# Kernel tuning notes

Hardware: AMD Instinct MI355X
Metric: run time of the kernel (lower is better)

Reference implementation:

```python
import jax, jax.numpy as jnp
import numpy as np

N_NODES = 50000
N_EDGES = 800000
NUM_RELS = 16
IN_DIM = 16      # == NUM_RELS (one-hot of op_class_id)
H_DIM = 128
OUT_DIM = 128    # must equal H_DIM (actor/critic consume output-layer root feats)
LIN_DIM = 512


def setup_inputs() -> dict:
    key = jax.random.key(0)
    ks = jax.random.split(key, 16)
    op_class_id = jax.random.randint(ks[0], (N_NODES,), 0, NUM_RELS, dtype=jnp.int32)
    norm = jax.random.uniform(ks[1], (N_NODES,), dtype=jnp.float32)
    src = jax.random.randint(ks[2], (N_EDGES,), 0, N_NODES, dtype=jnp.int32)
    dst = jax.random.randint(ks[3], (N_EDGES,), 0, N_NODES, dtype=jnp.int32)
    s = 0.1
    W0 = jax.random.normal(ks[4], (NUM_RELS, IN_DIM, H_DIM), jnp.float32) * s
    W1 = jax.random.normal(ks[5], (NUM_RELS, H_DIM, H_DIM), jnp.float32) * s
    W2 = jax.random.normal(ks[6], (NUM_RELS, H_DIM, OUT_DIM), jnp.float32) * s
    a1_w = jax.random.normal(ks[7], (OUT_DIM, LIN_DIM), jnp.float32) * s
    a1_b = jnp.zeros((LIN_DIM,), jnp.float32)
    a2_w = jax.random.normal(ks[8], (LIN_DIM, OUT_DIM), jnp.float32) * s
    a2_b = jnp.zeros((OUT_DIM,), jnp.float32)
    c1_w = jax.random.normal(ks[9], (OUT_DIM, LIN_DIM), jnp.float32) * s
    c1_b = jnp.zeros((LIN_DIM,), jnp.float32)
    c2_w = jax.random.normal(ks[10], (LIN_DIM, 1), jnp.float32) * s
    c2_b = jnp.zeros((1,), jnp.float32)
    return dict(op_class_id=op_class_id, norm=norm, src=src, dst=dst,
                W0=W0, W1=W1, W2=W2,
                a1_w=a1_w, a1_b=a1_b, a2_w=a2_w, a2_b=a2_b,
                c1_w=c1_w, c1_b=c1_b, c2_w=c2_w, c2_b=c2_b)


def _rgcn_layer(h, cls, norm, src, dst, W, act):
    # per-node relation-specific transform: h[n] @ W[cls[n]]
    # compute all relations then select (R small, avoids [N,in,out] gather)
    stacked = jnp.einsum('ni,rio->rno', h, W)          # [R, N, out]
    msg = stacked[cls, jnp.arange(h.shape[0])]         # [N, out]
    msg = msg * norm[:, None]
    agg = jax.ops.segment_sum(msg[src], dst, num_segments=h.shape[0])
    return act(agg)


def reference(op_class_id, norm, src, dst, W0, W1, W2,
              a1_w, a1_b, a2_w, a2_b, c1_w, c1_b, c2_w, c2_b):
    one_hot = jax.nn.one_hot(op_class_id, IN_DIM, dtype=jnp.float32)  # op_class_one_hot
    h = _rgcn_layer(one_hot, op_class_id, norm, src, dst, W0, jax.nn.relu)
    h = _rgcn_layer(h, op_class_id, norm, src, dst, W1, jax.nn.relu)
    h = _rgcn_layer(h, op_class_id, norm, src, dst, W2,
                    lambda x: jax.nn.softmax(x, axis=1))
    root = h[0]                                        # [OUT_DIM]
    probs = jax.nn.relu(root @ a1_w + a1_b) @ a2_w + a2_b
    value = jax.nn.relu(root @ c1_w + c1_b) @ c2_w + c2_b
    return probs, value
```

## Files before the change

kernel.cpp:

```cpp
#include <hip/hip_runtime.h>

#define NN 50000
#define NE 800000
#define NQ (NE / 4)
#define NR 16
#define HD 128
#define LIND 512

#define E0CAP 4096
#define SEGN 16
#define SEGCAP 2048
#define S1MAX 64
#define BMW 1600

#define PZ ((int)0xAAAAAAAA)

#define CNT(i) cnt[(i) * 16]
#define L_E0      0
#define L_E1(s)   (1 + (s))
#define L_SCAN(s) (17 + (s))
#define L_EDGE(s) (33 + (s))
#define L_DONE    49

#define NEB 256
#define NTB (NEB + NR + 16)

__global__ void k_scanA(const int* __restrict__ src, const int* __restrict__ dst,
                        int* map1, int* e0_src, int* cnt, int* map0bm) {
    int tid = blockIdx.x * blockDim.x + threadIdx.x;
    if (tid >= NQ) {
        int idx = tid - NQ;
        if (idx < BMW) map0bm[idx] = 0;
        return;
    }
    int4 d4 = ((const int4*)dst)[tid];
    int ds[4] = {d4.x, d4.y, d4.z, d4.w};
    #pragma unroll
    for (int j = 0; j < 4; j++) {
        if (ds[j] == 0) {
            int s = src[4 * tid + j];
            int i = atomicAdd(&CNT(L_E0), 1) - PZ;
            if (i >= 0 && i < E0CAP) e0_src[i] = s;
            map1[s] = 1;
        }
    }
}

__global__ void k_scanB1(const int* __restrict__ src, const int* __restrict__ dst,
                         const int* __restrict__ cls, const float* __restrict__ norm,
                         const int* __restrict__ map1, const int* __restrict__ e0_src,
                         int* map0bm, int4* e1seg, int* cnt) {
    __shared__ int s1l[S1MAX];
    int e0n = CNT(L_E0) - PZ;
    if (e0n < 0) e0n = 0; if (e0n > E0CAP) e0n = E0CAP;
    const int s1n = (e0n <= S1MAX) ? e0n : 0;
    if (threadIdx.x < s1n) s1l[threadIdx.x] = e0_src[threadIdx.x];
    __syncthreads();
    int tid = blockIdx.x * blockDim.x + threadIdx.x;
    if (tid >= NQ) return;
    int seg = blockIdx.x & (SEGN - 1);
    int4 d4 = ((const int4*)dst)[tid];
    int ds[4] = {d4.x, d4.y, d4.z, d4.w};
    #pragma unroll
    for (int j = 0; j < 4; j++) {
        int dv = ds[j];
        bool hit;
        if (s1n) {
            hit = false;
            for (int s2 = 0; s2 < s1n; s2++) hit |= (dv == s1l[s2]);
        } else {
            hit = (map1[dv] == 1);
        }
        if (hit) {
            int s = src[4 * tid + j];
            int i = atomicAdd(&CNT(L_E1(seg)), 1) - PZ;
            if (i >= 0 && i < SEGCAP)
                e1seg[seg * SEGCAP + i] =
                    make_int4(s, dv, cls[s], __float_as_int(norm[s]));
            atomicOr(&map0bm[s >> 5], 1 << (s & 31));
        }
    }
}

__global__ void __launch_bounds__(256, 2)
k_tail6(const int* __restrict__ src, const int* __restrict__ dst,
        const int* __restrict__ cls, const float* __restrict__ norm,
        const int* __restrict__ map0bm, int* cnt,
        const int* __restrict__ e0_src, const int4* __restrict__ e1seg,
        float* w0sum, float* agg1, float* rootpre,
        const float* __restrict__ W0, const float* __restrict__ W1,
        const float* __restrict__ W2,
        const float* __restrict__ a1w, const float* __restrict__ a1b,
        const float* __restrict__ a2w, const float* __restrict__ a2b,
        const float* __restrict__ c1w, const float* __restrict__ c1b,
        const float* __restrict__ c2w, const float* __restrict__ c2b,
        float* out) {
    const int t = threadIdx.x;
    const int b = blockIdx.x;

    __shared__ union {
        int bm[BMW];
        struct { float shw[NR]; float sha[HD]; float red[256]; } ed;
        struct { float u[HD]; int si[256]; int sc[256]; float sn[256]; int any; } rt;
        struct { float sha[HD]; float shz[64]; float red[256]; } mlp;
    } sm;

    {
        for (int i = t; i < BMW; i += 256) sm.bm[i] = map0bm[i];
        __syncthreads();
        const int4* d4p = (const int4*)dst;
        for (int q = b * 256 + t; q < NQ; q += NTB * 256) {
            int4 d4 = d4p[q];
            int ds[4] = {d4.x, d4.y, d4.z, d4.w};
            #pragma unroll
            for (int j = 0; j < 4; j++) {
                int dv = ds[j];
                if ((sm.bm[dv >> 5] >> (dv & 31)) & 1) {
                    int s = src[4 * q + j];
                    atomicAdd(&w0sum[((size_t)dv << 4) + cls[s]], norm[s]);
                }
            }
        }
    }
    __syncthreads();
    if (t == 0)
        __hip_atomic_fetch_add(&CNT(L_SCAN(b & (SEGN - 1))), 1,
                               __ATOMIC_RELAXED, __HIP_MEMORY_SCOPE_AGENT);

    if (b < NEB) {
        const int seg = b & (SEGN - 1);
        const int own = b >> 4;
        int len = CNT(L_E1(seg)) - PZ;
        if (len < 0) len = 0; if (len > SEGCAP) len = SEGCAP;
        const int o = t & 127, hf = t >> 7, kk0 = hf << 6;
        int u = 0, v = 0, c = 0; float nm = 0.f;
        float w1reg[64];
        float w0reg[NR];
        if (t < HD) {
            #pragma unroll
            for (int cc = 0; cc < NR; cc++) w0reg[cc] = W0[cc * 2176 + t];
        }
        bool have = (own < len);
        if (have) {
            int4 e = e1seg[seg * SEGCAP + own];
            u = e.x; v = e.y; c = e.z; nm = __int_as_float(e.w);
            const float* w = W1 + c * (HD * HD) + o;
            #pragma unroll
            for (int k = 0; k < 64; k++) w1reg[k] = w[(kk0 + k) << 7];
        }
        if (t == 0) {
            for (;;) {
                int tot = 0;
                #pragma unroll
                for (int s2 = 0; s2 < SEGN; s2++)
                    tot += __hip_atomic_load(&CNT(L_SCAN(s2)), __ATOMIC_RELAXED,
                                             __HIP_MEMORY_SCOPE_AGENT) - PZ;
                if (tot >= NTB) break;
                __builtin_amdgcn_s_sleep(1);
            }
        }
        __syncthreads();
        for (int i = own; i < len; i += NEB / SEGN) {
            if (i != own) {
                int4 e = e1seg[seg * SEGCAP + i];
                u = e.x; v = e.y; c = e.z; nm = __int_as_float(e.w);
                const float* w = W1 + c * (HD * HD) + o;
                #pragma unroll
                for (int k = 0; k < 64; k++) w1reg[k] = w[(kk0 + k) << 7];
            }
            if (t < NR)
                sm.ed.shw[t] = __hip_atomic_load(&w0sum[((size_t)u << 4) + t],
                                                 __ATOMIC_RELAXED,
                                                 __HIP_MEMORY_SCOPE_AGENT);
            __syncthreads();
            if (t < HD) {
                float a = 0.f;
                #pragma unroll
                for (int cc = 0; cc < NR; cc++) a = fmaf(sm.ed.shw[cc], w0reg[cc], a);
                sm.ed.sha[t] = fmaxf(a, 0.f);
            }
            __syncthreads();
            {
                float acc = 0.f;
                #pragma unroll
                for (int k = 0; k < 64; k++)
                    acc = fmaf(sm.ed.sha[kk0 + k], w1reg[k], acc);
                sm.ed.red[t] = acc;
            }
            __syncthreads();
            if (t < HD)
                atomicAdd(&agg1[((size_t)v << 7) + t],
                          (sm.ed.red[t] + sm.ed.red[t + 128]) * nm);
            __syncthreads();
        }
        __syncthreads();
        if (t == 0)
            __hip_atomic_fetch_add(&CNT(L_EDGE(seg)), 1,
                                   __ATOMIC_RELAXED, __HIP_MEMORY_SCOPE_AGENT);
    } else if (b < NEB + NR) {
        const int c = b - NEB;
        const int o = t & 127, hf = t >> 7, kk0 = hf << 6;
        if (t < HD) sm.rt.u[t] = 0.f;
        if (t == 0) sm.rt.any = 0;
        int e0n = CNT(L_E0) - PZ;
        if (e0n < 0) e0n = 0; if (e0n > E0CAP) e0n = E0CAP;
        if (t < e0n && t < 256) {
            int s0 = e0_src[t];
            sm.rt.si[t] = s0; sm.rt.sc[t] = cls[s0]; sm.rt.sn[t] = norm[s0];
        }
        float w2reg[64];
        {
            const float* w2 = W2 + c * (HD * HD) + o;
            #pragma unroll
            for (int k = 0; k < 64; k++) w2reg[k] = w2[(kk0 + k) << 7];
        }
        __syncthreads();
        if (t == 0) {
            for (;;) {
                int tot = 0;
                #pragma unroll
                for (int s2 = 0; s2 < SEGN; s2++)
                    tot += __hip_atomic_load(&CNT(L_EDGE(s2)), __ATOMIC_RELAXED,
                                             __HIP_MEMORY_SCOPE_AGENT) - PZ;
                if (tot >= NEB) break;
                __builtin_amdgcn_s_sleep(1);
            }
        }
        __syncthreads();
        for (int base = 0; base < e0n; base += 256) {
            int nchunk = e0n - base; if (nchunk > 256) nchunk = 256;
            if (base > 0) {
                if (t < nchunk) {
                    int s0 = e0_src[base + t];
                    sm.rt.si[t] = s0; sm.rt.sc[t] = cls[s0]; sm.rt.sn[t] = norm[s0];
                }
                __syncthreads();
            }
            for (int i = 0; i < nchunk; i++) {
                if (sm.rt.sc[i] != c) continue;
                if (t < HD) {
                    float av = __hip_atomic_load(&agg1[((size_t)sm.rt.si[i] << 7) + t],
                                                 __ATOMIC_RELAXED,
                                                 __HIP_MEMORY_SCOPE_AGENT);
                    sm.rt.u[t] += sm.rt.sn[i] * fmaxf(av, 0.f);
                }
                if (t == 0) sm.rt.any = 1;
            }
            __syncthreads();
        }
        if (sm.rt.any) {
            float acc = 0.f;
            #pragma unroll
            for (int k = 0; k < 64; k++) acc = fmaf(sm.rt.u[kk0 + k], w2reg[k], acc);
            atomicAdd(&rootpre[o], acc);
        }
        __syncthreads();
        if (t == 0)
            __hip_atomic_fetch_add(&CNT(L_DONE), 1,
                                   __ATOMIC_RELEASE, __HIP_MEMORY_SCOPE_AGENT);
    } else {
        const int bb = b - NEB - NR;
        const int m = bb >> 3, g = bb & 7, k0 = g << 6;
        const float* Wh = m ? c1w : a1w;
        const float* bh = m ? c1b : a1b;
        const int o1 = t & 63, qu = t >> 6, kk1 = qu << 5;
        float wreg[32];
        #pragma unroll
        for (int i = 0; i < 32; i++) wreg[i] = Wh[(kk1 + i) * LIND + k0 + o1];
        float breg = bh[k0 + o1];
        const int o2 = t & 127, hf2 = t >> 7, j2 = hf2 << 5;
        float vreg[32];
        if (m == 0) {
            #pragma unroll
            for (int j = 0; j < 32; j++) vreg[j] = a2w[(k0 + j2 + j) * HD + o2];
        } else {
            vreg[0] = c2w[k0 + o1];
        }
        if (t == 0) {
            while (__hip_atomic_load(&CNT(L_DONE), __ATOMIC_ACQUIRE,
                                     __HIP_MEMORY_SCOPE_AGENT) - PZ < NR)
                __builtin_amdgcn_s_sleep(2);
        }
        __syncthreads();
        if (t < HD)
            sm.mlp.sha[t] = __hip_atomic_load(&rootpre[t], __ATOMIC_RELAXED,
                                              __HIP_MEMORY_SCOPE_AGENT);
        __syncthreads();
        float mx = -3.0e38f;
        for (int i = 0; i < HD; i++) mx = fmaxf(mx, sm.mlp.sha[i]);
        float ex = (t < HD) ? expf(sm.mlp.sha[t] - mx) : 0.f;
        __syncthreads();
        if (t < HD) sm.mlp.sha[t] = ex;
        __syncthreads();
        float sum = 0.f;
        for (int i = 0; i < HD; i++) sum += sm.mlp.sha[i];
        __syncthreads();
        if (t < HD) sm.mlp.sha[t] = ex / sum;
        __syncthreads();
        {
            float z = 0.f;
            #pragma unroll
            for (int i = 0; i < 32; i++) z = fmaf(sm.mlp.sha[kk1 + i], wreg[i], z);
            sm.mlp.red[t] = z;
            __syncthreads();
            if (t < 64)
                sm.mlp.shz[t] = fmaxf(breg + sm.mlp.red[t] + sm.mlp.red[t + 64]
                                      + sm.mlp.red[t + 128] + sm.mlp.red[t + 192], 0.f);
        }
        __syncthreads();
        if (m == 0) {
            float acc = 0.f;
            #pragma unroll
            for (int j = 0; j < 32; j++) acc = fmaf(sm.mlp.shz[j2 + j], vreg[j], acc);
            sm.mlp.red[t] = acc;
            __syncthreads();
            if (t < HD) {
                float v = sm.mlp.red[t] + sm.mlp.red[t + 128];
                if (bb == 0) v += a2b[t];
                atomicAdd(&out[t], v);
            }
        } else {
            if (t < 64) sm.mlp.red[t] = sm.mlp.shz[t] * vreg[0];
            __syncthreads();
            if (t == 0) {
                float v = (bb == 8) ? c2b[0] : 0.f;
                for (int j = 0; j < 64; j++) v += sm.mlp.red[j];
                atomicAdd(&out[HD], v);
            }
        }
    }
}

extern "C" void kernel_launch(void* const* d_in, const int* in_sizes, int n_in,
                              void* d_out, int out_size, void* d_ws, size_t ws_size,
                              hipStream_t stream) {
    const int*   cls  = (const int*)d_in[0];
    const float* norm = (const float*)d_in[1];
    const int*   src  = (const int*)d_in[2];
    const int*   dst  = (const int*)d_in[3];
    const float* W0   = (const float*)d_in[4];
    const float* W1   = (const float*)d_in[5];
    const float* W2   = (const float*)d_in[6];
    const float* a1w  = (const float*)d_in[7];
    const float* a1b  = (const float*)d_in[8];
    const float* a2w  = (const float*)d_in[9];
    const float* a2b  = (const float*)d_in[10];
    const float* c1w  = (const float*)d_in[11];
    const float* c1b  = (const float*)d_in[12];
    const float* c2w  = (const float*)d_in[13];
    const float* c2b  = (const float*)d_in[14];
    float* out = (float*)d_out;

    char*  ws      = (char*)d_ws;
    int*   cnt     = (int*)(ws + 0);
    int*   e0_src  = (int*)(ws + 4096);
    float* rootpre = (float*)(ws + 20480);
    int*   map0bm  = (int*)(ws + 24576);
    int4*  e1seg   = (int4*)(ws + 32768);
    int*   map1    = (int*)(ws + 589824);
    float* w0sum   = (float*)(ws + 1048576);
    float* agg1    = (float*)(ws + 8388608);

    k_scanA<<<1024, 256, 0, stream>>>(src, dst, map1, e0_src, cnt, map0bm);
    k_scanB1<<<1024, 256, 0, stream>>>(src, dst, cls, norm, map1, e0_src,
                                       map0bm, e1seg, cnt);
    k_tail6<<<NTB, 256, 0, stream>>>(src, dst, cls, norm, map0bm, cnt, e0_src, e1seg,
                                     w0sum, agg1, rootpre, W0, W1, W2,
                                     a1w, a1b, a2w, a2b, c1w, c1b, c2w, c2b, out);
}
```

Before: 115.3 us.

## Fuse three kernel launches into one persistent kernel with grid-wide barriers

Merges the two scan kernels into the persistent tail kernel, replacing launch boundaries with counter-based grid barriers between phases. Each thread loads its dst quads into registers once and reuses them across all three scan phases. Each block rebuilds the layer-0 bitmap in shared memory from the edge list instead of reading a global bitmap. The edge records are split into two 64-bit arrays so they can be written and read with atomics. This removes launch overhead and the repeated dst reads, but the three scan passes now run on only 288 blocks instead of 1024, and it adds three barrier spins.

Measured after the change: 130.3 us. 1.13x slower.

```diff
diff --git a/kernel.cpp b/kernel.cpp
--- a/kernel.cpp
+++ b/kernel.cpp
@@ -18,132 +18,175 @@
 #define CNT(i) cnt[(i) * 16]
 #define L_E0      0
 #define L_E1(s)   (1 + (s))
-#define L_SCAN(s) (17 + (s))
-#define L_EDGE(s) (33 + (s))
-#define L_DONE    49
+#define L_P0(s)   (17 + (s))
+#define L_P1(s)   (33 + (s))
+#define L_P2(s)   (49 + (s))
+#define L_EDGE(s) (65 + (s))
+#define L_DONE    81
 
 #define NEB 256
 #define NTB (NEB + NR + 16)
-
-__global__ void k_scanA(const int* __restrict__ src, const int* __restrict__ dst,
-                        int* map1, int* e0_src, int* cnt, int* map0bm) {
-    int tid = blockIdx.x * blockDim.x + threadIdx.x;
-    if (tid >= NQ) {
-        int idx = tid - NQ;
-        if (idx < BMW) map0bm[idx] = 0;
-        return;
-    }
-    int4 d4 = ((const int4*)dst)[tid];
-    int ds[4] = {d4.x, d4.y, d4.z, d4.w};
-    #pragma unroll
-    for (int j = 0; j < 4; j++) {
-        if (ds[j] == 0) {
-            int s = src[4 * tid + j];
-            int i = atomicAdd(&CNT(L_E0), 1) - PZ;
-            if (i >= 0 && i < E0CAP) e0_src[i] = s;
-            map1[s] = 1;
-        }
-    }
+#define THRD (NTB * 256)
+
+typedef unsigned long long u64;
+#define ALOAD(p)    __hip_atomic_load((p), __ATOMIC_RELAXED, __HIP_MEMORY_SCOPE_AGENT)
+#define ASTORE(p,v) __hip_atomic_store((p), (v), __ATOMIC_RELAXED, __HIP_MEMORY_SCOPE_AGENT)
+__device__ __forceinline__ u64 pk2(int lo, int hi) {
+    return (u64)(unsigned)lo | ((u64)(unsigned)hi << 32);
 }
 
-__global__ void k_scanB1(const int* __restrict__ src, const int* __restrict__ dst,
-                         const int* __restrict__ cls, const float* __restrict__ norm,
-                         const int* __restrict__ map1, const int* __restrict__ e0_src,
-                         int* map0bm, int4* e1seg, int* cnt) {
-    __shared__ int s1l[S1MAX];
-    int e0n = CNT(L_E0) - PZ;
-    if (e0n < 0) e0n = 0; if (e0n > E0CAP) e0n = E0CAP;
-    const int s1n = (e0n <= S1MAX) ? e0n : 0;
-    if (threadIdx.x < s1n) s1l[threadIdx.x] = e0_src[threadIdx.x];
-    __syncthreads();
-    int tid = blockIdx.x * blockDim.x + threadIdx.x;
-    if (tid >= NQ) return;
-    int seg = blockIdx.x & (SEGN - 1);
-    int4 d4 = ((const int4*)dst)[tid];
-    int ds[4] = {d4.x, d4.y, d4.z, d4.w};
-    #pragma unroll
-    for (int j = 0; j < 4; j++) {
-        int dv = ds[j];
-        bool hit;
-        if (s1n) {
-            hit = false;
-            for (int s2 = 0; s2 < s1n; s2++) hit |= (dv == s1l[s2]);
-        } else {
-            hit = (map1[dv] == 1);
-        }
-        if (hit) {
-            int s = src[4 * tid + j];
-            int i = atomicAdd(&CNT(L_E1(seg)), 1) - PZ;
-            if (i >= 0 && i < SEGCAP)
-                e1seg[seg * SEGCAP + i] =
-                    make_int4(s, dv, cls[s], __float_as_int(norm[s]));
-            atomicOr(&map0bm[s >> 5], 1 << (s & 31));
-        }
-    }
-}
-
 __global__ void __launch_bounds__(256, 2)
-k_tail6(const int* __restrict__ src, const int* __restrict__ dst,
-        const int* __restrict__ cls, const float* __restrict__ norm,
-        const int* __restrict__ map0bm, int* cnt,
-        const int* __restrict__ e0_src, const int4* __restrict__ e1seg,
-        float* w0sum, float* agg1, float* rootpre,
-        const float* __restrict__ W0, const float* __restrict__ W1,
-        const float* __restrict__ W2,
-        const float* __restrict__ a1w, const float* __restrict__ a1b,
-        const float* __restrict__ a2w, const float* __restrict__ a2b,
-        const float* __restrict__ c1w, const float* __restrict__ c1b,
-        const float* __restrict__ c2w, const float* __restrict__ c2b,
-        float* out) {
+k_one(const int* __restrict__ src, const int* __restrict__ dst,
+      const int* __restrict__ cls, const float* __restrict__ norm,
+      int* cnt, int* e0_src, int* map1, u64* e1A, u64* e1B,
+      float* w0sum, float* agg1, float* rootpre,
+      const float* __restrict__ W0, const float* __restrict__ W1,
+      const float* __restrict__ W2,
+      const float* __restrict__ a1w, const float* __restrict__ a1b,
+      const float* __restrict__ a2w, const float* __restrict__ a2b,
+      const float* __restrict__ c1w, const float* __restrict__ c1b,
+      const float* __restrict__ c2w, const float* __restrict__ c2b,
+      float* out) {
     const int t = threadIdx.x;
     const int b = blockIdx.x;
+    const int tid = b * 256 + t;
+    const int seg = b & (SEGN - 1);
 
     __shared__ union {
         int bm[BMW];
+        int s1l[S1MAX];
         struct { float shw[NR]; float sha[HD]; float red[256]; } ed;
         struct { float u[HD]; int si[256]; int sc[256]; float sn[256]; int any; } rt;
         struct { float sha[HD]; float shz[64]; float red[256]; } mlp;
     } sm;
 
-    {
-        for (int i = t; i < BMW; i += 256) sm.bm[i] = map0bm[i];
-        __syncthreads();
-        const int4* d4p = (const int4*)dst;
-        for (int q = b * 256 + t; q < NQ; q += NTB * 256) {
-            int4 d4 = d4p[q];
-            int ds[4] = {d4.x, d4.y, d4.z, d4.w};
-            #pragma unroll
-            for (int j = 0; j < 4; j++) {
-                int dv = ds[j];
-                if ((sm.bm[dv >> 5] >> (dv & 31)) & 1) {
-                    int s = src[4 * q + j];
-                    atomicAdd(&w0sum[((size_t)dv << 4) + cls[s]], norm[s]);
+    const int4* d4p = (const int4*)dst;
+    int4 d4c[3];
+    #pragma unroll
+    for (int k = 0; k < 3; k++) {
+        int q = tid + k * THRD;
+        if (q < NQ) d4c[k] = d4p[q];
+    }
+    #pragma unroll
+    for (int k = 0; k < 3; k++) {
+        int q = tid + k * THRD;
+        if (q >= NQ) continue;
+        int ds[4] = {d4c[k].x, d4c[k].y, d4c[k].z, d4c[k].w};
+        #pragma unroll
+        for (int j = 0; j < 4; j++) {
+            if (ds[j] == 0) {
+                int s = src[4 * q + j];
+                int i = atomicAdd(&CNT(L_E0), 1) - PZ;
+                if (i >= 0 && i < E0CAP) ASTORE(&e0_src[i], s);
+                ASTORE(&map1[s], 1);
+            }
+        }
+    }
+    __syncthreads();
+    if (t == 0)
+        __hip_atomic_fetch_add(&CNT(L_P0(seg)), 1, __ATOMIC_RELAXED, __HIP_MEMORY_SCOPE_AGENT);
+    if (t == 0) {
+        for (;;) {
+            int tot = 0;
+            #pragma unroll
+            for (int s2 = 0; s2 < SEGN; s2++) tot += ALOAD(&CNT(L_P0(s2))) - PZ;
+            if (tot >= NTB) break;
+            __builtin_amdgcn_s_sleep(1);
+        }
+    }
+    __syncthreads();
+
+    int e0n = ALOAD(&CNT(L_E0)) - PZ;
+    if (e0n < 0) e0n = 0; if (e0n > E0CAP) e0n = E0CAP;
+    const int s1n = (e0n <= S1MAX) ? e0n : 0;
+    if (t < s1n) sm.s1l[t] = ALOAD(&e0_src[t]);
+    __syncthreads();
+    #pragma unroll
+    for (int k = 0; k < 3; k++) {
+        int q = tid + k * THRD;
+        if (q >= NQ) continue;
+        int ds[4] = {d4c[k].x, d4c[k].y, d4c[k].z, d4c[k].w};
+        #pragma unroll
+        for (int j = 0; j < 4; j++) {
+            int dv = ds[j];
+            bool hit;
+            if (s1n) {
+                hit = false;
+                for (int s2 = 0; s2 < s1n; s2++) hit |= (dv == sm.s1l[s2]);
+            } else {
+                hit = (ALOAD(&map1[dv]) == 1);
+            }
+            if (hit) {
+                int s = src[4 * q + j];
+                int i = atomicAdd(&CNT(L_E1(seg)), 1) - PZ;
+                if (i >= 0 && i < SEGCAP) {
+                    ASTORE(&e1A[seg * SEGCAP + i], pk2(s, dv));
+                    ASTORE(&e1B[seg * SEGCAP + i],
+                           pk2(cls[s], __float_as_int(norm[s])));
                 }
             }
         }
     }
     __syncthreads();
     if (t == 0)
-        __hip_atomic_fetch_add(&CNT(L_SCAN(b & (SEGN - 1))), 1,
-                               __ATOMIC_RELAXED, __HIP_MEMORY_SCOPE_AGENT);
+        __hip_atomic_fetch_add(&CNT(L_P1(seg)), 1, __ATOMIC_RELAXED, __HIP_MEMORY_SCOPE_AGENT);
+    if (t == 0) {
+        for (;;) {
+            int tot = 0;
+            #pragma unroll
+            for (int s2 = 0; s2 < SEGN; s2++) tot += ALOAD(&CNT(L_P1(s2))) - PZ;
+            if (tot >= NTB) break;
+            __builtin_amdgcn_s_sleep(1);
+        }
+    }
+    __syncthreads();
+
+    for (int i = t; i < BMW; i += 256) sm.bm[i] = 0;
+    __syncthreads();
+    for (int s2 = 0; s2 < SEGN; s2++) {
+        int len = ALOAD(&CNT(L_E1(s2))) - PZ;
+        if (len < 0) len = 0; if (len > SEGCAP) len = SEGCAP;
+        for (int i = t; i < len; i += 256) {
+            int s = (int)(ALOAD(&e1A[s2 * SEGCAP + i]) & 0xffffffffu);
+            atomicOr(&sm.bm[s >> 5], 1 << (s & 31));
+        }
+    }
+    __syncthreads();
+    #pragma unroll
+    for (int k = 0; k < 3; k++) {
+        int q = tid + k * THRD;
+        if (q >= NQ) continue;
+        int ds[4] = {d4c[k].x, d4c[k].y, d4c[k].z, d4c[k].w};
+        #pragma unroll
+        for (int j = 0; j < 4; j++) {
+            int dv = ds[j];
+            if ((sm.bm[dv >> 5] >> (dv & 31)) & 1) {
+                int s = src[4 * q + j];
+                atomicAdd(&w0sum[((size_t)dv << 4) + cls[s]], norm[s]);
+            }
+        }
+    }
+    __syncthreads();
+    if (t == 0)
+        __hip_atomic_fetch_add(&CNT(L_P2(seg)), 1, __ATOMIC_RELAXED, __HIP_MEMORY_SCOPE_AGENT);
 
     if (b < NEB) {
-        const int seg = b & (SEGN - 1);
         const int own = b >> 4;
-        int len = CNT(L_E1(seg)) - PZ;
+        int len = ALOAD(&CNT(L_E1(seg))) - PZ;
         if (len < 0) len = 0; if (len > SEGCAP) len = SEGCAP;
         const int o = t & 127, hf = t >> 7, kk0 = hf << 6;
+        float w0reg[NR];
+        if (t < HD) {
+            #pragma unroll
+            for (int cc = 0; cc < NR; cc++) w0reg[cc] = W0[cc * 2176 + t];
+        }
         int u = 0, v = 0, c = 0; float nm = 0.f;
         float w1reg[64];
-        float w0reg[NR];
-        if (t < HD) {
-            #pragma unroll
-            for (int cc = 0; cc < NR; cc++) w0reg[cc] = W0[cc * 2176 + t];
-        }
-        bool have = (own < len);
-        if (have) {
-            int4 e = e1seg[seg * SEGCAP + own];
-            u = e.x; v = e.y; c = e.z; nm = __int_as_float(e.w);
+        if (own < len) {
+            u64 ea = ALOAD(&e1A[seg * SEGCAP + own]);
+            u64 eb = ALOAD(&e1B[seg * SEGCAP + own]);
+            u = (int)(ea & 0xffffffffu); v = (int)(ea >> 32);
+            c = (int)(eb & 0xffffffffu); nm = __int_as_float((int)(eb >> 32));
             const float* w = W1 + c * (HD * HD) + o;
             #pragma unroll
             for (int k = 0; k < 64; k++) w1reg[k] = w[(kk0 + k) << 7];
@@ -152,9 +195,7 @@
             for (;;) {
                 int tot = 0;
                 #pragma unroll
-                for (int s2 = 0; s2 < SEGN; s2++)
-                    tot += __hip_atomic_load(&CNT(L_SCAN(s2)), __ATOMIC_RELAXED,
-                                             __HIP_MEMORY_SCOPE_AGENT) - PZ;
+                for (int s2 = 0; s2 < SEGN; s2++) tot += ALOAD(&CNT(L_P2(s2))) - PZ;
                 if (tot >= NTB) break;
                 __builtin_amdgcn_s_sleep(1);
             }
@@ -162,16 +203,17 @@
         __syncthreads();
         for (int i = own; i < len; i += NEB / SEGN) {
             if (i != own) {
-                int4 e = e1seg[seg * SEGCAP + i];
-                u = e.x; v = e.y; c = e.z; nm = __int_as_float(e.w);
+                u64 ea = ALOAD(&e1A[seg * SEGCAP + i]);
+                u64 eb = ALOAD(&e1B[seg * SEGCAP + i]);
+                u = (int)(ea & 0xffffffffu); v = (int)(ea >> 32);
+                c = (int)(eb & 0xffffffffu); nm = __int_as_float((int)(eb >> 32));
                 const float* w = W1 + c * (HD * HD) + o;
                 #pragma unroll
                 for (int k = 0; k < 64; k++) w1reg[k] = w[(kk0 + k) << 7];
             }
             if (t < NR)
                 sm.ed.shw[t] = __hip_atomic_load(&w0sum[((size_t)u << 4) + t],
-                                                 __ATOMIC_RELAXED,
-                                                 __HIP_MEMORY_SCOPE_AGENT);
+                                                 __ATOMIC_RELAXED, __HIP_MEMORY_SCOPE_AGENT);
             __syncthreads();
             if (t < HD) {
                 float a = 0.f;
@@ -183,8 +225,7 @@
             {
                 float acc = 0.f;
                 #pragma unroll
-                for (int k = 0; k < 64; k++)
-                    acc = fmaf(sm.ed.sha[kk0 + k], w1reg[k], acc);
+                for (int k = 0; k < 64; k++) acc = fmaf(sm.ed.sha[kk0 + k], w1reg[k], acc);
                 sm.ed.red[t] = acc;
             }
             __syncthreads();
@@ -195,17 +236,14 @@
         }
         __syncthreads();
         if (t == 0)
-            __hip_atomic_fetch_add(&CNT(L_EDGE(seg)), 1,
-                                   __ATOMIC_RELAXED, __HIP_MEMORY_SCOPE_AGENT);
+            __hip_atomic_fetch_add(&CNT(L_EDGE(seg)), 1, __ATOMIC_RELAXED, __HIP_MEMORY_SCOPE_AGENT);
     } else if (b < NEB + NR) {
         const int c = b - NEB;
         const int o = t & 127, hf = t >> 7, kk0 = hf << 6;
         if (t < HD) sm.rt.u[t] = 0.f;
         if (t == 0) sm.rt.any = 0;
-        int e0n = CNT(L_E0) - PZ;
-        if (e0n < 0) e0n = 0; if (e0n > E0CAP) e0n = E0CAP;
         if (t < e0n && t < 256) {
-            int s0 = e0_src[t];
+            int s0 = ALOAD(&e0_src[t]);
             sm.rt.si[t] = s0; sm.rt.sc[t] = cls[s0]; sm.rt.sn[t] = norm[s0];
         }
         float w2reg[64];
@@ -219,9 +257,7 @@
             for (;;) {
                 int tot = 0;
                 #pragma unroll
-                for (int s2 = 0; s2 < SEGN; s2++)
-                    tot += __hip_atomic_load(&CNT(L_EDGE(s2)), __ATOMIC_RELAXED,
-                                             __HIP_MEMORY_SCOPE_AGENT) - PZ;
+                for (int s2 = 0; s2 < SEGN; s2++) tot += ALOAD(&CNT(L_EDGE(s2))) - PZ;
                 if (tot >= NEB) break;
                 __builtin_amdgcn_s_sleep(1);
             }
@@ -231,7 +267,7 @@
             int nchunk = e0n - base; if (nchunk > 256) nchunk = 256;
             if (base > 0) {
                 if (t < nchunk) {
-                    int s0 = e0_src[base + t];
+                    int s0 = ALOAD(&e0_src[base + t]);
                     sm.rt.si[t] = s0; sm.rt.sc[t] = cls[s0]; sm.rt.sn[t] = norm[s0];
                 }
                 __syncthreads();
@@ -240,8 +276,7 @@
                 if (sm.rt.sc[i] != c) continue;
                 if (t < HD) {
                     float av = __hip_atomic_load(&agg1[((size_t)sm.rt.si[i] << 7) + t],
-                                                 __ATOMIC_RELAXED,
-                                                 __HIP_MEMORY_SCOPE_AGENT);
+                                                 __ATOMIC_RELAXED, __HIP_MEMORY_SCOPE_AGENT);
                     sm.rt.u[t] += sm.rt.sn[i] * fmaxf(av, 0.f);
                 }
                 if (t == 0) sm.rt.any = 1;
@@ -256,8 +291,7 @@
         }
         __syncthreads();
         if (t == 0)
-            __hip_atomic_fetch_add(&CNT(L_DONE), 1,
-                                   __ATOMIC_RELEASE, __HIP_MEMORY_SCOPE_AGENT);
+            __hip_atomic_fetch_add(&CNT(L_DONE), 1, __ATOMIC_RELEASE, __HIP_MEMORY_SCOPE_AGENT);
     } else {
         const int bb = b - NEB - NR;
         const int m = bb >> 3, g = bb & 7, k0 = g << 6;
@@ -353,18 +387,15 @@
 
     char*  ws      = (char*)d_ws;
     int*   cnt     = (int*)(ws + 0);
-    int*   e0_src  = (int*)(ws + 4096);
-    float* rootpre = (float*)(ws + 20480);
-    int*   map0bm  = (int*)(ws + 24576);
-    int4*  e1seg   = (int4*)(ws + 32768);
-    int*   map1    = (int*)(ws + 589824);
+    int*   e0_src  = (int*)(ws + 8192);
+    float* rootpre = (float*)(ws + 24576);
+    int*   map1    = (int*)(ws + 32768);
+    u64*   e1A     = (u64*)(ws + 262144);
+    u64*   e1B     = (u64*)(ws + 524288);
     float* w0sum   = (float*)(ws + 1048576);
     float* agg1    = (float*)(ws + 8388608);
 
-    k_scanA<<<1024, 256, 0, stream>>>(src, dst, map1, e0_src, cnt, map0bm);
-    k_scanB1<<<1024, 256, 0, stream>>>(src, dst, cls, norm, map1, e0_src,
-                                       map0bm, e1seg, cnt);
-    k_tail6<<<NTB, 256, 0, stream>>>(src, dst, cls, norm, map0bm, cnt, e0_src, e1seg,
-                                     w0sum, agg1, rootpre, W0, W1, W2,
-                                     a1w, a1b, a2w, a2b, c1w, c1b, c2w, c2b, out);
+    k_one<<<NTB, 256, 0, stream>>>(src, dst, cls, norm, cnt, e0_src, map1,
+                                   e1A, e1B, w0sum, agg1, rootpre, W0, W1, W2,
+                                   a1w, a1b, a2w, a2b, c1w, c1b, c2w, c2b, out);
 }
```

## Split w0sum scan into separate kernel, removing in-kernel grid barrier

Applied to the files above, without the earlier changes.

Moves the third full edge scan (accumulating w0sum for nodes in the 2-hop frontier) out of the persistent tail kernel into its own 1024-block kernel. Each block rebuilds the frontier bitmap in shared memory from the e1seg lists instead of using a global atomicOr bitmap. The spin-wait barrier is removed, and the scan now runs across many more blocks. The trade-off is an extra kernel launch, plus every block redundantly reading the e1seg lists to rebuild the bitmap.

Measured after the change: 116.0 us. No clear change (+0.7%).

```diff
diff --git a/kernel.cpp b/kernel.cpp
--- a/kernel.cpp
+++ b/kernel.cpp
@@ -18,21 +18,16 @@
 #define CNT(i) cnt[(i) * 16]
 #define L_E0      0
 #define L_E1(s)   (1 + (s))
-#define L_SCAN(s) (17 + (s))
-#define L_EDGE(s) (33 + (s))
-#define L_DONE    49
+#define L_EDGE(s) (17 + (s))
+#define L_DONE    33
 
 #define NEB 256
 #define NTB (NEB + NR + 16)
 
 __global__ void k_scanA(const int* __restrict__ src, const int* __restrict__ dst,
-                        int* map1, int* e0_src, int* cnt, int* map0bm) {
+                        int* map1, int* e0_src, int* cnt) {
     int tid = blockIdx.x * blockDim.x + threadIdx.x;
-    if (tid >= NQ) {
-        int idx = tid - NQ;
-        if (idx < BMW) map0bm[idx] = 0;
-        return;
-    }
+    if (tid >= NQ) return;
     int4 d4 = ((const int4*)dst)[tid];
     int ds[4] = {d4.x, d4.y, d4.z, d4.w};
     #pragma unroll
@@ -49,7 +44,7 @@
 __global__ void k_scanB1(const int* __restrict__ src, const int* __restrict__ dst,
                          const int* __restrict__ cls, const float* __restrict__ norm,
                          const int* __restrict__ map1, const int* __restrict__ e0_src,
-                         int* map0bm, int4* e1seg, int* cnt) {
+                         int4* e1seg, int* cnt) {
     __shared__ int s1l[S1MAX];
     int e0n = CNT(L_E0) - PZ;
     if (e0n < 0) e0n = 0; if (e0n > E0CAP) e0n = E0CAP;
@@ -77,17 +72,44 @@
             if (i >= 0 && i < SEGCAP)
                 e1seg[seg * SEGCAP + i] =
                     make_int4(s, dv, cls[s], __float_as_int(norm[s]));
-            atomicOr(&map0bm[s >> 5], 1 << (s & 31));
+        }
+    }
+}
+
+__global__ void k_scanB2(const int* __restrict__ src, const int* __restrict__ dst,
+                         const int* __restrict__ cls, const float* __restrict__ norm,
+                         const int4* __restrict__ e1seg, const int* __restrict__ cnt,
+                         float* w0sum) {
+    __shared__ int bm[BMW];
+    for (int i = threadIdx.x; i < BMW; i += 256) bm[i] = 0;
+    __syncthreads();
+    for (int s2 = 0; s2 < SEGN; s2++) {
+        int len = CNT(L_E1(s2)) - PZ;
+        if (len < 0) len = 0; if (len > SEGCAP) len = SEGCAP;
+        for (int i = threadIdx.x; i < len; i += 256) {
+            int s = e1seg[s2 * SEGCAP + i].x;
+            atomicOr(&bm[s >> 5], 1 << (s & 31));
+        }
+    }
+    __syncthreads();
+    int tid = blockIdx.x * blockDim.x + threadIdx.x;
+    if (tid >= NQ) return;
+    int4 d4 = ((const int4*)dst)[tid];
+    int ds[4] = {d4.x, d4.y, d4.z, d4.w};
+    #pragma unroll
+    for (int j = 0; j < 4; j++) {
+        int dv = ds[j];
+        if ((bm[dv >> 5] >> (dv & 31)) & 1) {
+            int s = src[4 * tid + j];
+            atomicAdd(&w0sum[((size_t)dv << 4) + cls[s]], norm[s]);
         }
     }
 }
 
 __global__ void __launch_bounds__(256, 2)
-k_tail6(const int* __restrict__ src, const int* __restrict__ dst,
-        const int* __restrict__ cls, const float* __restrict__ norm,
-        const int* __restrict__ map0bm, int* cnt,
-        const int* __restrict__ e0_src, const int4* __restrict__ e1seg,
-        float* w0sum, float* agg1, float* rootpre,
+k_tail7(const int* __restrict__ cls, const float* __restrict__ norm,
+        int* cnt, const int* __restrict__ e0_src, const int4* __restrict__ e1seg,
+        const float* __restrict__ w0sum, float* agg1, float* rootpre,
         const float* __restrict__ W0, const float* __restrict__ W1,
         const float* __restrict__ W2,
         const float* __restrict__ a1w, const float* __restrict__ a1b,
@@ -99,33 +121,10 @@
     const int b = blockIdx.x;
 
     __shared__ union {
-        int bm[BMW];
         struct { float shw[NR]; float sha[HD]; float red[256]; } ed;
         struct { float u[HD]; int si[256]; int sc[256]; float sn[256]; int any; } rt;
         struct { float sha[HD]; float shz[64]; float red[256]; } mlp;
     } sm;
-
-    {
-        for (int i = t; i < BMW; i += 256) sm.bm[i] = map0bm[i];
-        __syncthreads();
-        const int4* d4p = (const int4*)dst;
-        for (int q = b * 256 + t; q < NQ; q += NTB * 256) {
-            int4 d4 = d4p[q];
-            int ds[4] = {d4.x, d4.y, d4.z, d4.w};
-            #pragma unroll
-            for (int j = 0; j < 4; j++) {
-                int dv = ds[j];
-                if ((sm.bm[dv >> 5] >> (dv & 31)) & 1) {
-                    int s = src[4 * q + j];
-                    atomicAdd(&w0sum[((size_t)dv << 4) + cls[s]], norm[s]);
-                }
-            }
-        }
-    }
-    __syncthreads();
-    if (t == 0)
-        __hip_atomic_fetch_add(&CNT(L_SCAN(b & (SEGN - 1))), 1,
-                               __ATOMIC_RELAXED, __HIP_MEMORY_SCOPE_AGENT);
 
     if (b < NEB) {
         const int seg = b & (SEGN - 1);
@@ -133,45 +132,20 @@
         int len = CNT(L_E1(seg)) - PZ;
         if (len < 0) len = 0; if (len > SEGCAP) len = SEGCAP;
         const int o = t & 127, hf = t >> 7, kk0 = hf << 6;
-        int u = 0, v = 0, c = 0; float nm = 0.f;
-        float w1reg[64];
         float w0reg[NR];
         if (t < HD) {
             #pragma unroll
             for (int cc = 0; cc < NR; cc++) w0reg[cc] = W0[cc * 2176 + t];
         }
-        bool have = (own < len);
-        if (have) {
-            int4 e = e1seg[seg * SEGCAP + own];
-            u = e.x; v = e.y; c = e.z; nm = __int_as_float(e.w);
+        for (int i = own; i < len; i += NEB / SEGN) {
+            int4 e = e1seg[seg * SEGCAP + i];
+            int u = e.x, v = e.y, c = e.z;
+            float nm = __int_as_float(e.w);
             const float* w = W1 + c * (HD * HD) + o;
+            float w1reg[64];
             #pragma unroll
             for (int k = 0; k < 64; k++) w1reg[k] = w[(kk0 + k) << 7];
-        }
-        if (t == 0) {
-            for (;;) {
-                int tot = 0;
-                #pragma unroll
-                for (int s2 = 0; s2 < SEGN; s2++)
-                    tot += __hip_atomic_load(&CNT(L_SCAN(s2)), __ATOMIC_RELAXED,
-                                             __HIP_MEMORY_SCOPE_AGENT) - PZ;
-                if (tot >= NTB) break;
-                __builtin_amdgcn_s_sleep(1);
-            }
-        }
-        __syncthreads();
-        for (int i = own; i < len; i += NEB / SEGN) {
-            if (i != own) {
-                int4 e = e1seg[seg * SEGCAP + i];
-                u = e.x; v = e.y; c = e.z; nm = __int_as_float(e.w);
-                const float* w = W1 + c * (HD * HD) + o;
-                #pragma unroll
-                for (int k = 0; k < 64; k++) w1reg[k] = w[(kk0 + k) << 7];
-            }
-            if (t < NR)
-                sm.ed.shw[t] = __hip_atomic_load(&w0sum[((size_t)u << 4) + t],
-                                                 __ATOMIC_RELAXED,
-                                                 __HIP_MEMORY_SCOPE_AGENT);
+            if (t < NR) sm.ed.shw[t] = w0sum[((size_t)u << 4) + t];
             __syncthreads();
             if (t < HD) {
                 float a = 0.f;
@@ -183,8 +157,7 @@
             {
                 float acc = 0.f;
                 #pragma unroll
-                for (int k = 0; k < 64; k++)
-                    acc = fmaf(sm.ed.sha[kk0 + k], w1reg[k], acc);
+                for (int k = 0; k < 64; k++) acc = fmaf(sm.ed.sha[kk0 + k], w1reg[k], acc);
                 sm.ed.red[t] = acc;
             }
             __syncthreads();
@@ -355,16 +328,15 @@
     int*   cnt     = (int*)(ws + 0);
     int*   e0_src  = (int*)(ws + 4096);
     float* rootpre = (float*)(ws + 20480);
-    int*   map0bm  = (int*)(ws + 24576);
     int4*  e1seg   = (int4*)(ws + 32768);
     int*   map1    = (int*)(ws + 589824);
     float* w0sum   = (float*)(ws + 1048576);
     float* agg1    = (float*)(ws + 8388608);
 
-    k_scanA<<<1024, 256, 0, stream>>>(src, dst, map1, e0_src, cnt, map0bm);
-    k_scanB1<<<1024, 256, 0, stream>>>(src, dst, cls, norm, map1, e0_src,
-                                       map0bm, e1seg, cnt);
-    k_tail6<<<NTB, 256, 0, stream>>>(src, dst, cls, norm, map0bm, cnt, e0_src, e1seg,
+    k_scanA<<<1024, 256, 0, stream>>>(src, dst, map1, e0_src, cnt);
+    k_scanB1<<<1024, 256, 0, stream>>>(src, dst, cls, norm, map1, e0_src, e1seg, cnt);
+    k_scanB2<<<1024, 256, 0, stream>>>(src, dst, cls, norm, e1seg, cnt, w0sum);
+    k_tail7<<<NTB, 256, 0, stream>>>(cls, norm, cnt, e0_src, e1seg,
                                      w0sum, agg1, rootpre, W0, W1, W2,
                                      a1w, a1b, a2w, a2b, c1w, c1b, c2w, c2b, out);
 }
```
